# Optimization experiments

Hardware: AMD Instinct MI355X
Metric: run time of the kernel (lower is better)

Reference implementation:

```python
import jax, jax.numpy as jnp
import numpy as np

N, E, D = 100000, 400000, 128

def setup_inputs() -> dict:
    key = jax.random.key(0)
    k1, k2, k3, k4, k5 = jax.random.split(key, 5)
    x = jax.random.normal(k1, (N, D), dtype=jnp.float32)
    e = jax.random.normal(k2, (E, D), dtype=jnp.float32)
    # torch nn.Linear(3D, D, bias=False) weight is [D, 3D]; we store W = weight.T -> [3D, D]
    W = jax.random.normal(k3, (3 * D, D), dtype=jnp.float32) * (1.0 / np.sqrt(3 * D))
    src_idx = jax.random.randint(k4, (E,), 0, N, dtype=jnp.int64)
    dst_idx = jax.random.randint(k5, (E,), 0, N, dtype=jnp.int64)
    return {"x": x, "e": e, "W": W, "src_idx": src_idx, "dst_idx": dst_idx}

def reference(x, e, W, src_idx, dst_idx):
    # message = Linear(concat([src_feat, tgt_feat, role_feat], -1))
    # Split W into the three d-blocks so we never materialize the [E, 3D] concat:
    # concat([a,b,c]) @ W == a@W1 + b@W2 + c@W3  (exactly the same math)
    d = x.shape[-1]
    W_src, W_dst, W_e = W[:d], W[d:2 * d], W[2 * d:]
    m = x[src_idx] @ W_src + x[dst_idx] @ W_dst + e @ W_e  # [E, D]
    return m
```

## Files before the change

### kernel.cpp

```cpp
#include <hip/hip_runtime.h>
#include <hip/hip_bf16.h>

typedef __attribute__((ext_vector_type(8))) short bf16x8;
typedef __attribute__((ext_vector_type(4))) float f32x4;

#define D128 128
#define IMG_SHORTS 16384
#define XB_OFF 65536
#define NBLK 256
#define WSH (3 * IMG_SHORTS)
#define RBS 4096

__device__ __forceinline__ short f2bf(float f) {
    union { float f; unsigned u; } v; v.f = f;
    unsigned r = (v.u + 0x7FFFu + ((v.u >> 16) & 1u)) >> 16;
    return (short)r;
}

__device__ __forceinline__ short f2bf_h(float f) {
    __hip_bfloat16 h = __float2bfloat16(f);
    short s;
    __builtin_memcpy(&s, &h, sizeof(short));
    return s;
}

__device__ __forceinline__ bf16x8 pack8(f32x4 a, f32x4 b) {
    bf16x8 r;
    r[0] = f2bf_h(a[0]); r[1] = f2bf_h(a[1]); r[2] = f2bf_h(a[2]); r[3] = f2bf_h(a[3]);
    r[4] = f2bf_h(b[0]); r[5] = f2bf_h(b[1]); r[6] = f2bf_h(b[2]); r[7] = f2bf_h(b[3]);
    return r;
}

__device__ __forceinline__ void gload_lds16(const short* g, short* l) {
    __builtin_amdgcn_global_load_lds(
        (const __attribute__((address_space(1))) unsigned int*)(const void*)g,
        (__attribute__((address_space(3))) unsigned int*)(void*)l, 16, 0, 0);
}

__global__ __launch_bounds__(256) void wt_kernel(const float* __restrict__ W,
                                                 short* __restrict__ Wimg) {
    const int c    = blockIdx.x >> 3;
    const int frag = (blockIdx.x & 7) * 4 + (threadIdx.x >> 6);
    const int lane = threadIdx.x & 63;
    const int mt = frag >> 2, ks = frag & 3;
    const int m  = mt * 16 + (lane & 15);
    const int k0 = ks * 32 + (lane >> 4) * 8;
    bf16x8 v;
#pragma unroll
    for (int j = 0; j < 8; ++j)
        v[j] = f2bf(W[(size_t)(c * 128 + k0 + j) * D128 + m]);
    *reinterpret_cast<bf16x8*>(
        &Wimg[((size_t)c * 32 + frag) * 64 * 8 + (size_t)lane * 8]) = v;
}

__global__ __launch_bounds__(256) void xb_kernel(const float* __restrict__ x,
                                                 short* __restrict__ xb) {
    const size_t i = ((size_t)blockIdx.x * 256 + threadIdx.x) * 8;
    f32x4 v0 = reinterpret_cast<const f32x4*>(x + i)[0];
    f32x4 v1 = reinterpret_cast<const f32x4*>(x + i)[1];
    *reinterpret_cast<bf16x8*>(xb + i) = pack8(v0, v1);
}

__global__ __launch_bounds__(512, 2) void fused_kernel(
        const short* __restrict__ xb,
        const float* __restrict__ e,
        const short* __restrict__ Wimg,
        const int*  __restrict__ src_idx,
        const int*  __restrict__ dst_idx,
        float* __restrict__ out,
        int E, int ntiles)
{
    __shared__ short lds[WSH + 8 * RBS];

    const int tid  = threadIdx.x;
    const int lane = tid & 63;
    const int w    = tid >> 6;
    const int r    = lane >> 2;
    const int q    = lane & 3;
    const int sx   = (r >> 1) & 3;
    const int fr   = lane & 15;
    const int lhi  = lane >> 4;
    const int rb_off = (fr * 4 + (lhi ^ ((fr >> 1) & 3))) * 8;

    short* RB = &lds[WSH + w * RBS];

    const int per = ntiles >> 8;
    const int rem = ntiles & 255;
    const int b   = blockIdx.x;
    const int t0  = b * per + (b < rem ? b : rem);
    const int t1  = t0 + per + (b < rem ? 1 : 0);

#pragma unroll
    for (int jj = 0; jj < 12; ++jj) {
        int unit = jj * 512 + tid;
        gload_lds16(Wimg + (size_t)unit * 8, &lds[unit * 8]);
    }
    int rp = t0 * 128 + w * 16 + r;
    int si = src_idx[rp];
    int di = dst_idx[rp];
    asm volatile("" ::: "memory");
    asm volatile("s_waitcnt vmcnt(0)" ::: "memory");
    __builtin_amdgcn_s_barrier();

#pragma unroll
    for (int ks = 0; ks < 4; ++ks)
        gload_lds16(xb + (size_t)si * D128 + ks * 32 + (q ^ sx) * 8, &RB[ks * 512]);
    asm volatile("" ::: "memory");

    for (int t = t0; t < t1; ++t) {
        const int rn = t * 128 + w * 16 + fr;

#pragma unroll
        for (int ks = 0; ks < 4; ++ks)
            gload_lds16(xb + (size_t)di * D128 + ks * 32 + (q ^ sx) * 8,
                        &RB[2048 + ks * 512]);
        asm volatile("" ::: "memory");

        const float* pe = e + (size_t)rn * D128;
        f32x4 ev[8];
#pragma unroll
        for (int ks = 0; ks < 4; ++ks) {
            ev[2 * ks]     = reinterpret_cast<const f32x4*>(pe + ks * 32 + lhi * 8)[0];
            ev[2 * ks + 1] = reinterpret_cast<const f32x4*>(pe + ks * 32 + lhi * 8)[1];
        }
        asm volatile("" ::: "memory");

        int rpn = (t + 1) * 128 + w * 16 + r;
        if (rpn >= E) rpn = E - 1;
        const int sin_ = src_idx[rpn];
        const int din_ = dst_idx[rpn];
        asm volatile("" ::: "memory");

        asm volatile("s_waitcnt vmcnt(14)" ::: "memory");
        __builtin_amdgcn_sched_barrier(0);

        f32x4 acc[8];
#pragma unroll
        for (int mt = 0; mt < 8; ++mt) acc[mt] = (f32x4){0.f, 0.f, 0.f, 0.f};

#pragma unroll
        for (int ks = 0; ks < 4; ++ks) {
            bf16x8 bfr = *reinterpret_cast<const bf16x8*>(&RB[ks * 512 + rb_off]);
#pragma unroll
            for (int mt = 0; mt < 8; ++mt) {
                bf16x8 a = *reinterpret_cast<const bf16x8*>(
                    &lds[((0 * 32 + mt * 4 + ks) * 64 + lane) * 8]);
                acc[mt] = __builtin_amdgcn_mfma_f32_16x16x32_bf16(a, bfr, acc[mt], 0, 0, 0);
            }
        }

        asm volatile("s_waitcnt vmcnt(10)" ::: "memory");
        __builtin_amdgcn_sched_barrier(0);

#pragma unroll
        for (int ks = 0; ks < 4; ++ks) {
            bf16x8 bfr = *reinterpret_cast<const bf16x8*>(&RB[2048 + ks * 512 + rb_off]);
#pragma unroll
            for (int mt = 0; mt < 8; ++mt) {
                bf16x8 a = *reinterpret_cast<const bf16x8*>(
                    &lds[((1 * 32 + mt * 4 + ks) * 64 + lane) * 8]);
                acc[mt] = __builtin_amdgcn_mfma_f32_16x16x32_bf16(a, bfr, acc[mt], 0, 0, 0);
            }
        }
        asm volatile("" ::: "memory");

#pragma unroll
        for (int ks = 0; ks < 4; ++ks)
            gload_lds16(xb + (size_t)sin_ * D128 + ks * 32 + (q ^ sx) * 8, &RB[ks * 512]);
        asm volatile("" ::: "memory");
        si = sin_; di = din_;

        asm volatile("s_waitcnt vmcnt(6)" ::: "memory");
        __builtin_amdgcn_sched_barrier(0);

        bf16x8 be[4];
#pragma unroll
        for (int ks = 0; ks < 4; ++ks) be[ks] = pack8(ev[2 * ks], ev[2 * ks + 1]);
#pragma unroll
        for (int ks = 0; ks < 4; ++ks)
#pragma unroll
            for (int mt = 0; mt < 8; ++mt) {
                bf16x8 a = *reinterpret_cast<const bf16x8*>(
                    &lds[((2 * 32 + mt * 4 + ks) * 64 + lane) * 8]);
                acc[mt] = __builtin_amdgcn_mfma_f32_16x16x32_bf16(a, be[ks], acc[mt], 0, 0, 0);
            }

        float* po = out + (size_t)rn * D128 + lhi * 4;
#pragma unroll
        for (int mt = 0; mt < 8; ++mt)
            *reinterpret_cast<f32x4*>(po + mt * 16) = acc[mt];
        asm volatile("" ::: "memory");
    }
}

extern "C" void kernel_launch(void* const* d_in, const int* in_sizes, int n_in,
                              void* d_out, int out_size, void* d_ws, size_t ws_size,
                              hipStream_t stream) {
    const float* x = (const float*)d_in[0];
    const float* e = (const float*)d_in[1];
    const float* W = (const float*)d_in[2];
    const int* src = (const int*)d_in[3];
    const int* dst = (const int*)d_in[4];
    float* out = (float*)d_out;

    short* Wimg = (short*)d_ws;
    short* xb   = (short*)d_ws + XB_OFF;

    const int N = in_sizes[0] / D128;
    const int E = in_sizes[3];
    const int ntiles = E / 128;

    wt_kernel<<<24, 256, 0, stream>>>(W, Wimg);
    xb_kernel<<<(N * D128) / (256 * 8), 256, 0, stream>>>(x, xb);
    fused_kernel<<<NBLK, 512, 0, stream>>>(xb, e, Wimg, src, dst, out, E, ntiles);
}
```

Measured before the change: 129.5 us.

## Stage e loads and output stores through LDS for coalesced row access

New measurement: 125.7 us (median of 2 runs). -2.9%, faster.

```diff
diff --git a/kernel.cpp b/kernel.cpp
--- a/kernel.cpp
+++ b/kernel.cpp
@@ -81,8 +81,13 @@
     const int fr   = lane & 15;
     const int lhi  = lane >> 4;
     const int rb_off = (fr * 4 + (lhi ^ ((fr >> 1) & 3))) * 8;
+    const int tw_w = ((r  & 1) << 2) ^ ((r  >> 1) & 3);
+    const int tw_r = ((fr & 1) << 2) ^ ((fr >> 1) & 3);
+    const int st_w = (fr * 4 + (lhi ^ ((fr >> 1) & 3))) * 8;
+    const int st_r = (r  * 4 + (q   ^ sx)) * 8;
 
     short* RB = &lds[WSH + w * RBS];
+    short* BB = RB + 2048;
 
     const int per = ntiles >> 8;
     const int rem = ntiles & 255;
@@ -108,21 +113,19 @@
     asm volatile("" ::: "memory");
 
     for (int t = t0; t < t1; ++t) {
-        const int rn = t * 128 + w * 16 + fr;
+        const int lrow = t * 128 + w * 16 + r;
 
 #pragma unroll
         for (int ks = 0; ks < 4; ++ks)
             gload_lds16(xb + (size_t)di * D128 + ks * 32 + (q ^ sx) * 8,
-                        &RB[2048 + ks * 512]);
-        asm volatile("" ::: "memory");
-
-        const float* pe = e + (size_t)rn * D128;
+                        &BB[ks * 512]);
+        asm volatile("" ::: "memory");
+
+        const float* pe = e + (size_t)lrow * D128;
         f32x4 ev[8];
 #pragma unroll
-        for (int ks = 0; ks < 4; ++ks) {
-            ev[2 * ks]     = reinterpret_cast<const f32x4*>(pe + ks * 32 + lhi * 8)[0];
-            ev[2 * ks + 1] = reinterpret_cast<const f32x4*>(pe + ks * 32 + lhi * 8)[1];
-        }
+        for (int j = 0; j < 8; ++j)
+            ev[j] = *reinterpret_cast<const f32x4*>(pe + (q + 4 * j) * 4);
         asm volatile("" ::: "memory");
 
         int rpn = (t + 1) * 128 + w * 16 + r;
@@ -154,7 +157,7 @@
 
 #pragma unroll
         for (int ks = 0; ks < 4; ++ks) {
-            bf16x8 bfr = *reinterpret_cast<const bf16x8*>(&RB[2048 + ks * 512 + rb_off]);
+            bf16x8 bfr = *reinterpret_cast<const bf16x8*>(&BB[ks * 512 + rb_off]);
 #pragma unroll
             for (int mt = 0; mt < 8; ++mt) {
                 bf16x8 a = *reinterpret_cast<const bf16x8*>(
@@ -173,23 +176,43 @@
         asm volatile("s_waitcnt vmcnt(6)" ::: "memory");
         __builtin_amdgcn_sched_barrier(0);
 
-        bf16x8 be[4];
-#pragma unroll
-        for (int ks = 0; ks < 4; ++ks) be[ks] = pack8(ev[2 * ks], ev[2 * ks + 1]);
-#pragma unroll
-        for (int ks = 0; ks < 4; ++ks)
-#pragma unroll
-            for (int mt = 0; mt < 8; ++mt) {
-                bf16x8 a = *reinterpret_cast<const bf16x8*>(
-                    &lds[((2 * 32 + mt * 4 + ks) * 64 + lane) * 8]);
-                acc[mt] = __builtin_amdgcn_mfma_f32_16x16x32_bf16(a, be[ks], acc[mt], 0, 0, 0);
-            }
-
-        float* po = out + (size_t)rn * D128 + lhi * 4;
-#pragma unroll
-        for (int mt = 0; mt < 8; ++mt)
-            *reinterpret_cast<f32x4*>(po + mt * 16) = acc[mt];
-        asm volatile("" ::: "memory");
+#pragma unroll
+        for (int R = 0; R < 2; ++R) {
+#pragma unroll
+            for (int jp = 0; jp < 4; ++jp) {
+                int slot = (q + 4 * jp) ^ tw_w;
+                *reinterpret_cast<f32x4*>(&BB[r * 128 + slot * 8]) = ev[R * 4 + jp];
+            }
+#pragma unroll
+            for (int ksl = 0; ksl < 2; ++ksl) {
+                const int ks = R * 2 + ksl;
+                const int u0 = ksl * 8 + lhi * 2;
+                f32x4 va = *reinterpret_cast<const f32x4*>(&BB[fr * 128 + (u0 ^ tw_r) * 8]);
+                f32x4 vb = *reinterpret_cast<const f32x4*>(&BB[fr * 128 + ((u0 + 1) ^ tw_r) * 8]);
+                bf16x8 be = pack8(va, vb);
+#pragma unroll
+                for (int mt = 0; mt < 8; ++mt) {
+                    bf16x8 a = *reinterpret_cast<const bf16x8*>(
+                        &lds[((2 * 32 + mt * 4 + ks) * 64 + lane) * 8]);
+                    acc[mt] = __builtin_amdgcn_mfma_f32_16x16x32_bf16(a, be, acc[mt], 0, 0, 0);
+                }
+            }
+        }
+
+        float* po = out + (size_t)lrow * D128 + q * 4;
+#pragma unroll
+        for (int R = 0; R < 2; ++R) {
+#pragma unroll
+            for (int p = 0; p < 4; ++p)
+                *reinterpret_cast<f32x4*>(&BB[p * 512 + st_w]) = acc[R * 4 + p];
+            asm volatile("" ::: "memory");
+#pragma unroll
+            for (int p = 0; p < 4; ++p) {
+                f32x4 v = *reinterpret_cast<const f32x4*>(&BB[p * 512 + st_r]);
+                *reinterpret_cast<f32x4*>(po + (R * 4 + p) * 16) = v;
+            }
+            asm volatile("" ::: "memory");
+        }
     }
 }
 
```
